# Kernel optimization log

Measured on AMD Instinct MI355X. Metric: run time of the kernel, lower is better.

## Reference

```python
import jax, jax.numpy as jnp
import numpy as np

B, T, I, H, FF, C = 4096, 512, 13, 7, 512, 1


def setup_inputs() -> dict:
    key = jax.random.key(0)
    ks = jax.random.split(key, 9)
    s_ih = 1.0 / np.sqrt(H)
    return {
        "x": jax.random.normal(ks[0], (B, T, I), dtype=jnp.float32),
        # PyTorch LSTM params, gate order i,f,g,o, uniform(-1/sqrt(H), 1/sqrt(H))
        "w_ih": jax.random.uniform(ks[1], (4 * H, I), minval=-s_ih, maxval=s_ih, dtype=jnp.float32),
        "w_hh": jax.random.uniform(ks[2], (4 * H, H), minval=-s_ih, maxval=s_ih, dtype=jnp.float32),
        "b_ih": jax.random.uniform(ks[3], (4 * H,), minval=-s_ih, maxval=s_ih, dtype=jnp.float32),
        "b_hh": jax.random.uniform(ks[4], (4 * H,), minval=-s_ih, maxval=s_ih, dtype=jnp.float32),
        "fc1_w": jax.random.uniform(ks[5], (FF, H), minval=-s_ih, maxval=s_ih, dtype=jnp.float32),
        "fc1_b": jax.random.uniform(ks[6], (FF,), minval=-s_ih, maxval=s_ih, dtype=jnp.float32),
        "fc_w": jax.random.uniform(ks[7], (C, FF), minval=-1.0 / np.sqrt(FF), maxval=1.0 / np.sqrt(FF), dtype=jnp.float32),
        "fc_b": jax.random.uniform(ks[8], (C,), minval=-1.0 / np.sqrt(FF), maxval=1.0 / np.sqrt(FF), dtype=jnp.float32),
    }


def _lstm_last_hidden(x, w_ih, w_hh, b_ih, b_hh):
    # Precompute input contributions for all timesteps: [B, T, 4H]
    xg = jnp.einsum("bti,gi->btg", x, w_ih) + b_ih

    def step(carry, xg_t):
        h, c = carry
        gates = xg_t + h @ w_hh.T + b_hh  # [B, 4H]
        i, f, g, o = jnp.split(gates, 4, axis=-1)
        i = jax.nn.sigmoid(i)
        f = jax.nn.sigmoid(f)
        g = jnp.tanh(g)
        o = jax.nn.sigmoid(o)
        c = f * c + i * g
        h = o * jnp.tanh(c)
        return (h, c), None

    h0 = jnp.zeros((x.shape[0], w_hh.shape[1]), dtype=x.dtype)
    (hn, _), _ = jax.lax.scan(step, (h0, h0), jnp.swapaxes(xg, 0, 1))
    return hn  # [B, H]


def reference(x, w_ih, w_hh, b_ih, b_hh, fc1_w, fc1_b, fc_w, fc_b):
    # Dropout(0.1) is identity in eval mode.
    hn = _lstm_last_hidden(x, w_ih, w_hh, b_ih, b_hh)
    out = jax.nn.relu(hn)
    out = jax.nn.relu(out @ fc1_w.T + fc1_b)
    return out @ fc_w.T + fc_b  # [B, 1]
```

## Files before the change

kernel.cpp:

```cpp
#include <hip/hip_runtime.h>

#define BB 4096
#define TN 512
#define IN 13
#define HN 7
#define FFD 512
#define CT 32
#define SC 8
#define NCK (TN / CT)
#define GPB 2

#define SWZ(v, imm) __int_as_float(__builtin_amdgcn_ds_swizzle(__float_as_int(v), (imm)))
#define QB(v, q)    __int_as_float(__builtin_amdgcn_mov_dpp(__float_as_int(v), (q)*0x55, 0xF, 0xF, true))

__global__ __launch_bounds__(64, 2)
void lstm_fused(const float* __restrict__ x,
                const float* __restrict__ w_ih,
                const float* __restrict__ w_hh,
                const float* __restrict__ b_ih,
                const float* __restrict__ b_hh,
                const float* __restrict__ fc1_w,
                const float* __restrict__ fc1_b,
                const float* __restrict__ fc_w,
                const float* __restrict__ fc_b,
                float* __restrict__ out)
{
    __shared__ float xs[2][GPB][CT][16];

    const int tid  = threadIdx.x;
    const int grp  = tid >> 5;
    const int lane = tid & 31;
    const int b    = blockIdx.x * GPB + grp;

    const int tau = lane & 3;
    const int ju  = lane >> 2;
    const int jj  = (ju < HN) ? ju : (HN - 1);
    const int row = tau * HN + jj;

    float wih[IN], whh[HN];
#pragma unroll
    for (int i = 0; i < IN; ++i) wih[i] = w_ih[row * IN + i];
#pragma unroll
    for (int k = 0; k < HN; ++k) whh[k] = w_hh[row * HN + k];
    const float bias = b_ih[row] + b_hh[row];

    const float L2E  = 1.4426950408889634f;
    const bool  is_tanh = (tau == 2);
    const float kmul = is_tanh ? (-2.0f * L2E) : (-L2E);
    const float sc   = is_tanh ?  2.0f : 1.0f;
    const float offc = is_tanh ? -1.0f : 0.0f;

    float h0 = 0.f, h1 = 0.f, h2 = 0.f, h3 = 0.f, h4 = 0.f, h5 = 0.f, h6 = 0.f;
    float cval = 0.0f;

    const float* xrow = x + ((long)b * TN + lane) * IN;

    {
        const float* src = xrow;
        float p[13];
#pragma unroll
        for (int i = 0; i < IN; ++i) p[i] = src[i];
        float* dst = &xs[0][grp][lane][0];
        *(float4*)(dst)     = make_float4(p[0], p[1], p[2],  p[3]);
        *(float4*)(dst + 4) = make_float4(p[4], p[5], p[6],  p[7]);
        *(float4*)(dst + 8) = make_float4(p[8], p[9], p[10], p[11]);
        dst[12] = p[12];
    }
    __syncthreads();

    for (int ck = 0; ck < NCK; ++ck) {
        const int cur = ck & 1;

        float p[13];
        const bool havenext = (ck + 1 < NCK);
        if (havenext) {
            const float* src = xrow + (ck + 1) * CT * IN;
#pragma unroll
            for (int i = 0; i < IN; ++i) p[i] = src[i];
        }

#pragma unroll
        for (int scb = 0; scb < CT / SC; ++scb) {
            float xdot[SC];
#pragma unroll
            for (int ss = 0; ss < SC; ++ss) {
                const float* xr = &xs[cur][grp][scb * SC + ss][0];
                const float4 a  = *(const float4*)(xr);
                const float4 b4 = *(const float4*)(xr + 4);
                const float4 c4 = *(const float4*)(xr + 8);
                const float  d0 = xr[12];
                float s0 = fmaf(wih[0], a.x, bias);
                s0 = fmaf(wih[1], a.y, s0);
                s0 = fmaf(wih[2], a.z, s0);
                s0 = fmaf(wih[3], a.w, s0);
                float s1 = wih[4] * b4.x;
                s1 = fmaf(wih[5], b4.y, s1);
                s1 = fmaf(wih[6], b4.z, s1);
                s1 = fmaf(wih[7], b4.w, s1);
                float s2 = wih[8] * c4.x;
                s2 = fmaf(wih[9],  c4.y, s2);
                s2 = fmaf(wih[10], c4.z, s2);
                s2 = fmaf(wih[11], c4.w, s2);
                s2 = fmaf(wih[12], d0,   s2);
                xdot[ss] = (s0 + s1) + s2;
            }

#pragma unroll
            for (int ss = 0; ss < SC; ++ss) {
                float s0 = fmaf(whh[0], h0, xdot[ss]);
                s0 = fmaf(whh[1], h1, s0);
                s0 = fmaf(whh[2], h2, s0);
                s0 = fmaf(whh[3], h3, s0);
                float s1 = whh[4] * h4;
                s1 = fmaf(whh[5], h5, s1);
                s1 = fmaf(whh[6], h6, s1);
                const float s = s0 + s1;

                float e   = __builtin_amdgcn_exp2f(kmul * s);
                float val = fmaf(__builtin_amdgcn_rcpf(1.0f + e), sc, offc);

                float iv = QB(val, 0);
                float fv = QB(val, 1);
                float gv = QB(val, 2);
                float ov = QB(val, 3);

                cval = fmaf(fv, cval, iv * gv);
                float e2 = __builtin_amdgcn_exp2f(-2.0f * L2E * cval);
                float th = fmaf(__builtin_amdgcn_rcpf(1.0f + e2), 2.0f, -1.0f);
                float hq = ov * th;

                h0 = SWZ(hq, (0  << 5));
                h1 = SWZ(hq, (4  << 5));
                h2 = SWZ(hq, (8  << 5));
                h3 = SWZ(hq, (12 << 5));
                h4 = SWZ(hq, (16 << 5));
                h5 = SWZ(hq, (20 << 5));
                h6 = SWZ(hq, (24 << 5));
            }
        }

        if (havenext) {
            float* dst = &xs[cur ^ 1][grp][lane][0];
            *(float4*)(dst)     = make_float4(p[0], p[1], p[2],  p[3]);
            *(float4*)(dst + 4) = make_float4(p[4], p[5], p[6],  p[7]);
            *(float4*)(dst + 8) = make_float4(p[8], p[9], p[10], p[11]);
            dst[12] = p[12];
        }
        __syncthreads();
    }

    float hb[HN] = { fmaxf(h0,0.f), fmaxf(h1,0.f), fmaxf(h2,0.f), fmaxf(h3,0.f),
                     fmaxf(h4,0.f), fmaxf(h5,0.f), fmaxf(h6,0.f) };

    float acc = 0.0f;
#pragma unroll
    for (int k = 0; k < FFD / 32; ++k) {
        int r = lane + (k << 5);
        float s = fc1_b[r];
#pragma unroll
        for (int j = 0; j < HN; ++j) s = fmaf(fc1_w[r * HN + j], hb[j], s);
        s = fmaxf(s, 0.0f);
        acc = fmaf(fc_w[r], s, acc);
    }
#pragma unroll
    for (int o = 16; o >= 1; o >>= 1) acc += __shfl_xor(acc, o, 32);
    if (lane == 0) out[b] = acc + fc_b[0];
}

extern "C" void kernel_launch(void* const* d_in, const int* in_sizes, int n_in,
                              void* d_out, int out_size, void* d_ws, size_t ws_size,
                              hipStream_t stream) {
    const float* x     = (const float*)d_in[0];
    const float* w_ih  = (const float*)d_in[1];
    const float* w_hh  = (const float*)d_in[2];
    const float* b_ih  = (const float*)d_in[3];
    const float* b_hh  = (const float*)d_in[4];
    const float* fc1_w = (const float*)d_in[5];
    const float* fc1_b = (const float*)d_in[6];
    const float* fc_w  = (const float*)d_in[7];
    const float* fc_b  = (const float*)d_in[8];
    float* out = (float*)d_out;

    dim3 grid(BB / GPB);
    dim3 block(64);
    hipLaunchKernelGGL(lstm_fused, grid, block, 0, stream,
                       x, w_ih, w_hh, b_ih, b_hh, fc1_w, fc1_b, fc_w, fc_b, out);
}
```

Baseline: 107.9 us.

## Split input projection and recurrence into producer and consumer wavefronts

Each block now has two wavefronts. One loads x chunks and computes the input-gate projections into a double-buffered LDS array. The other runs only the serial recurrent update, reading precomputed projections. This is meant to take the input projection work off the latency-bound recurrence wave so the two overlap. It doubles the threads per block and adds LDS traffic, and the producer reuses a scratch LDS buffer that relies on in-wave ordering without a barrier.

```diff
diff --git a/kernel.cpp b/kernel.cpp
--- a/kernel.cpp
+++ b/kernel.cpp
@@ -6,14 +6,13 @@
 #define HN 7
 #define FFD 512
 #define CT 32
-#define SC 8
 #define NCK (TN / CT)
 #define GPB 2
 
 #define SWZ(v, imm) __int_as_float(__builtin_amdgcn_ds_swizzle(__float_as_int(v), (imm)))
 #define QB(v, q)    __int_as_float(__builtin_amdgcn_mov_dpp(__float_as_int(v), (q)*0x55, 0xF, 0xF, true))
 
-__global__ __launch_bounds__(64, 2)
+__global__ __launch_bounds__(128, 4)
 void lstm_fused(const float* __restrict__ x,
                 const float* __restrict__ w_ih,
                 const float* __restrict__ w_hh,
@@ -25,11 +24,14 @@
                 const float* __restrict__ fc_b,
                 float* __restrict__ out)
 {
-    __shared__ float xs[2][GPB][CT][16];
+    __shared__ float xd[2][CT][64];
+    __shared__ float xs[GPB][CT][16];
 
     const int tid  = threadIdx.x;
-    const int grp  = tid >> 5;
-    const int lane = tid & 31;
+    const int wid  = tid >> 6;
+    const int l64  = tid & 63;
+    const int grp  = l64 >> 5;
+    const int lane = l64 & 31;
     const int b    = blockIdx.x * GPB + grp;
 
     const int tau = lane & 3;
@@ -37,14 +39,56 @@
     const int jj  = (ju < HN) ? ju : (HN - 1);
     const int row = tau * HN + jj;
 
-    float wih[IN], whh[HN];
+    const float L2E = 1.4426950408889634f;
+
+    float wih[IN];
+    float bias = 0.0f;
+    if (wid == 1) {
 #pragma unroll
-    for (int i = 0; i < IN; ++i) wih[i] = w_ih[row * IN + i];
+        for (int i = 0; i < IN; ++i) wih[i] = w_ih[row * IN + i];
+        bias = b_ih[row] + b_hh[row];
+    }
+
+    auto produce = [&](int ck) {
+        const float* src = x + ((long)b * TN + ck * CT + lane) * IN;
+        float p[IN];
 #pragma unroll
-    for (int k = 0; k < HN; ++k) whh[k] = w_hh[row * HN + k];
-    const float bias = b_ih[row] + b_hh[row];
+        for (int i = 0; i < IN; ++i) p[i] = src[i];
+        float* dst = &xs[grp][lane][0];
+        *(float4*)(dst)     = make_float4(p[0], p[1], p[2],  p[3]);
+        *(float4*)(dst + 4) = make_float4(p[4], p[5], p[6],  p[7]);
+        *(float4*)(dst + 8) = make_float4(p[8], p[9], p[10], p[11]);
+        dst[12] = p[12];
+        const int buf = ck & 1;
+#pragma unroll
+        for (int s = 0; s < CT; ++s) {
+            const float* xr = &xs[grp][s][0];
+            const float4 a  = *(const float4*)(xr);
+            const float4 b4 = *(const float4*)(xr + 4);
+            const float4 c4 = *(const float4*)(xr + 8);
+            const float  d0 = xr[12];
+            float s0 = fmaf(wih[0], a.x, bias);
+            s0 = fmaf(wih[1], a.y, s0);
+            s0 = fmaf(wih[2], a.z, s0);
+            s0 = fmaf(wih[3], a.w, s0);
+            float s1 = wih[4] * b4.x;
+            s1 = fmaf(wih[5], b4.y, s1);
+            s1 = fmaf(wih[6], b4.z, s1);
+            s1 = fmaf(wih[7], b4.w, s1);
+            float s2 = wih[8] * c4.x;
+            s2 = fmaf(wih[9],  c4.y, s2);
+            s2 = fmaf(wih[10], c4.z, s2);
+            s2 = fmaf(wih[11], c4.w, s2);
+            s2 = fmaf(wih[12], d0,   s2);
+            xd[buf][s][l64] = (s0 + s1) + s2;
+        }
+    };
 
-    const float L2E  = 1.4426950408889634f;
+    float whh[HN];
+    if (wid == 0) {
+#pragma unroll
+        for (int k = 0; k < HN; ++k) whh[k] = w_hh[row * HN + k];
+    }
     const bool  is_tanh = (tau == 2);
     const float kmul = is_tanh ? (-2.0f * L2E) : (-L2E);
     const float sc   = is_tanh ?  2.0f : 1.0f;
@@ -53,70 +97,30 @@
     float h0 = 0.f, h1 = 0.f, h2 = 0.f, h3 = 0.f, h4 = 0.f, h5 = 0.f, h6 = 0.f;
     float cval = 0.0f;
 
-    const float* xrow = x + ((long)b * TN + lane) * IN;
-
-    {
-        const float* src = xrow;
-        float p[13];
-#pragma unroll
-        for (int i = 0; i < IN; ++i) p[i] = src[i];
-        float* dst = &xs[0][grp][lane][0];
-        *(float4*)(dst)     = make_float4(p[0], p[1], p[2],  p[3]);
-        *(float4*)(dst + 4) = make_float4(p[4], p[5], p[6],  p[7]);
-        *(float4*)(dst + 8) = make_float4(p[8], p[9], p[10], p[11]);
-        dst[12] = p[12];
-    }
+    if (wid == 1) produce(0);
     __syncthreads();
 
     for (int ck = 0; ck < NCK; ++ck) {
-        const int cur = ck & 1;
-
-        float p[13];
-        const bool havenext = (ck + 1 < NCK);
-        if (havenext) {
-            const float* src = xrow + (ck + 1) * CT * IN;
+        if (wid == 1) {
+            if (ck + 1 < NCK) produce(ck + 1);
+        } else {
+            const int buf = ck & 1;
+            float xr[CT];
 #pragma unroll
-            for (int i = 0; i < IN; ++i) p[i] = src[i];
-        }
+            for (int s = 0; s < CT; ++s) xr[s] = xd[buf][s][l64];
 
 #pragma unroll
-        for (int scb = 0; scb < CT / SC; ++scb) {
-            float xdot[SC];
-#pragma unroll
-            for (int ss = 0; ss < SC; ++ss) {
-                const float* xr = &xs[cur][grp][scb * SC + ss][0];
-                const float4 a  = *(const float4*)(xr);
-                const float4 b4 = *(const float4*)(xr + 4);
-                const float4 c4 = *(const float4*)(xr + 8);
-                const float  d0 = xr[12];
-                float s0 = fmaf(wih[0], a.x, bias);
-                s0 = fmaf(wih[1], a.y, s0);
-                s0 = fmaf(wih[2], a.z, s0);
-                s0 = fmaf(wih[3], a.w, s0);
-                float s1 = wih[4] * b4.x;
-                s1 = fmaf(wih[5], b4.y, s1);
-                s1 = fmaf(wih[6], b4.z, s1);
-                s1 = fmaf(wih[7], b4.w, s1);
-                float s2 = wih[8] * c4.x;
-                s2 = fmaf(wih[9],  c4.y, s2);
-                s2 = fmaf(wih[10], c4.z, s2);
-                s2 = fmaf(wih[11], c4.w, s2);
-                s2 = fmaf(wih[12], d0,   s2);
-                xdot[ss] = (s0 + s1) + s2;
-            }
-
-#pragma unroll
-            for (int ss = 0; ss < SC; ++ss) {
-                float s0 = fmaf(whh[0], h0, xdot[ss]);
+            for (int s = 0; s < CT; ++s) {
+                float s0 = fmaf(whh[0], h0, xr[s]);
                 s0 = fmaf(whh[1], h1, s0);
                 s0 = fmaf(whh[2], h2, s0);
                 s0 = fmaf(whh[3], h3, s0);
                 float s1 = whh[4] * h4;
                 s1 = fmaf(whh[5], h5, s1);
                 s1 = fmaf(whh[6], h6, s1);
-                const float s = s0 + s1;
+                const float sg = s0 + s1;
 
-                float e   = __builtin_amdgcn_exp2f(kmul * s);
+                float e   = __builtin_amdgcn_exp2f(kmul * sg);
                 float val = fmaf(__builtin_amdgcn_rcpf(1.0f + e), sc, offc);
 
                 float iv = QB(val, 0);
@@ -138,16 +142,10 @@
                 h6 = SWZ(hq, (24 << 5));
             }
         }
-
-        if (havenext) {
-            float* dst = &xs[cur ^ 1][grp][lane][0];
-            *(float4*)(dst)     = make_float4(p[0], p[1], p[2],  p[3]);
-            *(float4*)(dst + 4) = make_float4(p[4], p[5], p[6],  p[7]);
-            *(float4*)(dst + 8) = make_float4(p[8], p[9], p[10], p[11]);
-            dst[12] = p[12];
-        }
         __syncthreads();
     }
+
+    if (wid == 1) return;
 
     float hb[HN] = { fmaxf(h0,0.f), fmaxf(h1,0.f), fmaxf(h2,0.f), fmaxf(h3,0.f),
                      fmaxf(h4,0.f), fmaxf(h5,0.f), fmaxf(h6,0.f) };
@@ -182,7 +180,7 @@
     float* out = (float*)d_out;
 
     dim3 grid(BB / GPB);
-    dim3 block(64);
+    dim3 block(128);
     hipLaunchKernelGGL(lstm_fused, grid, block, 0, stream,
                        x, w_ih, w_hh, b_ih, b_hh, fc1_w, fc1_b, fc_w, fc_b, out);
 }
```

Result: faster. 96.90 us (-10.2%).
